# Kernel optimization log

Measured on AMD Instinct MI355X. Metric: run time of the kernel, lower is better.

The kernel has to match this reference:

```python
import jax, jax.numpy as jnp
import numpy as np

N, D = 8192, 2
MIN_DIST = 0.1


def setup_inputs() -> dict:
    key = jax.random.key(0)
    k1, k2 = jax.random.split(key)
    predictions = jax.random.uniform(k1, (N, D), dtype=jnp.float32)
    targets = jax.random.uniform(k2, (N, D), dtype=jnp.float32)
    return {"predictions": predictions, "targets": targets}


def reference(predictions, targets):
    # primary loss: MSE (mean reduction), matching nn.MSELoss / F.mse_loss default
    primary_loss = jnp.mean(jnp.square(predictions - targets))

    # pairwise Euclidean distances via ||pi||^2 + ||pj||^2 - 2 pi.pj
    sq = jnp.sum(jnp.square(predictions), axis=-1)          # [N]
    d2 = sq[:, None] + sq[None, :] - 2.0 * (predictions @ predictions.T)  # [N, N]

    # only pairs with i < j contribute (strict upper triangle)
    mask = jnp.triu(jnp.ones((N, N), dtype=bool), k=1)
    d2 = jnp.where(mask, jnp.maximum(d2, 0.0), 1.0)  # dummy 1.0 keeps sqrt grad-safe
    dist = jnp.sqrt(d2)

    # penalty: (min_distance - d)^2 when d < min_distance, else 0
    pen = jnp.square(jnp.maximum(MIN_DIST - dist, 0.0))
    proximity_penalty = jnp.sum(jnp.where(mask, pen, 0.0))

    return primary_loss + proximity_penalty
```

## Files before the change

kernel.cpp:

```cpp
#include <hip/hip_runtime.h>

#define NPTS 8192
#define TILE 128
#define TT (NPTS / TILE)
#define NPAIRS (TT * (TT + 1) / 2)
#define MIN_DIST 0.1f

__global__ __launch_bounds__(64) void pair_tiles(const float2* __restrict__ P,
                                                 const float* __restrict__ pred,
                                                 const float* __restrict__ targ,
                                                 float* __restrict__ partial) {
    int k = blockIdx.x;

    int bi = (int)(((float)(2 * TT + 1) -
                    sqrtf((float)((2 * TT + 1) * (2 * TT + 1) - 8 * k))) * 0.5f);
    bi = min(max(bi, 0), TT - 1);
    while (bi > 0 && (bi * TT - bi * (bi - 1) / 2) > k) --bi;
    while (((bi + 1) * TT - (bi + 1) * bi / 2) <= k) ++bi;
    int bj = bi + (k - (bi * TT - bi * (bi - 1) / 2));
    bi = __builtin_amdgcn_readfirstlane(bi);
    bj = __builtin_amdgcn_readfirstlane(bj);

    int t = threadIdx.x;
    float2 a0 = P[bi * TILE + t];
    float2 a1 = P[bi * TILE + 64 + t];
    const float4* __restrict__ q4 = (const float4*)(P + bj * TILE);

    float acc = 0.0f;
    if (bi == bj) {
#pragma unroll 8
        for (int jj = 0; jj < TILE / 2; ++jj) {
            float4 q = q4[jj];
            float dx0 = a0.x - q.x, dy0 = a0.y - q.y;
            float dx1 = a0.x - q.z, dy1 = a0.y - q.w;
            float dx2 = a1.x - q.x, dy2 = a1.y - q.y;
            float dx3 = a1.x - q.z, dy3 = a1.y - q.w;
            float u0 = fmaxf(MIN_DIST - __builtin_amdgcn_sqrtf(fmaf(dy0, dy0, dx0 * dx0)), 0.0f);
            float u1 = fmaxf(MIN_DIST - __builtin_amdgcn_sqrtf(fmaf(dy1, dy1, dx1 * dx1)), 0.0f);
            float u2 = fmaxf(MIN_DIST - __builtin_amdgcn_sqrtf(fmaf(dy2, dy2, dx2 * dx2)), 0.0f);
            float u3 = fmaxf(MIN_DIST - __builtin_amdgcn_sqrtf(fmaf(dy3, dy3, dx3 * dx3)), 0.0f);
            u0 = (2 * jj == t) ? 0.0f : u0;
            u1 = (2 * jj + 1 == t) ? 0.0f : u1;
            u2 = (2 * jj == 64 + t) ? 0.0f : u2;
            u3 = (2 * jj + 1 == 64 + t) ? 0.0f : u3;
            acc = fmaf(u0, u0, acc);
            acc = fmaf(u1, u1, acc);
            acc = fmaf(u2, u2, acc);
            acc = fmaf(u3, u3, acc);
        }
        acc *= 0.5f;
    } else {
#pragma unroll 8
        for (int jj = 0; jj < TILE / 2; ++jj) {
            float4 q = q4[jj];
            float dx0 = a0.x - q.x, dy0 = a0.y - q.y;
            float dx1 = a0.x - q.z, dy1 = a0.y - q.w;
            float dx2 = a1.x - q.x, dy2 = a1.y - q.y;
            float dx3 = a1.x - q.z, dy3 = a1.y - q.w;
            float u0 = fmaxf(MIN_DIST - __builtin_amdgcn_sqrtf(fmaf(dy0, dy0, dx0 * dx0)), 0.0f);
            float u1 = fmaxf(MIN_DIST - __builtin_amdgcn_sqrtf(fmaf(dy1, dy1, dx1 * dx1)), 0.0f);
            float u2 = fmaxf(MIN_DIST - __builtin_amdgcn_sqrtf(fmaf(dy2, dy2, dx2 * dx2)), 0.0f);
            float u3 = fmaxf(MIN_DIST - __builtin_amdgcn_sqrtf(fmaf(dy3, dy3, dx3 * dx3)), 0.0f);
            acc = fmaf(u0, u0, acc);
            acc = fmaf(u1, u1, acc);
            acc = fmaf(u2, u2, acc);
            acc = fmaf(u3, u3, acc);
        }
    }

    if (k < 32) {
        int base = k * 128 + t;
        float4 p0 = ((const float4*)pred)[base];
        float4 r0 = ((const float4*)targ)[base];
        float4 p1 = ((const float4*)pred)[base + 64];
        float4 r1 = ((const float4*)targ)[base + 64];
        float e0 = p0.x - r0.x, e1 = p0.y - r0.y, e2 = p0.z - r0.z, e3 = p0.w - r0.w;
        float e4 = p1.x - r1.x, e5 = p1.y - r1.y, e6 = p1.z - r1.z, e7 = p1.w - r1.w;
        float m = e0 * e0;
        m = fmaf(e1, e1, m);
        m = fmaf(e2, e2, m);
        m = fmaf(e3, e3, m);
        m = fmaf(e4, e4, m);
        m = fmaf(e5, e5, m);
        m = fmaf(e6, e6, m);
        m = fmaf(e7, e7, m);
        acc = fmaf(m, 1.0f / 16384.0f, acc);
    }

    for (int off = 32; off > 0; off >>= 1)
        acc += __shfl_down(acc, off, 64);
    if (t == 0) partial[k] = acc;
}

__global__ __launch_bounds__(256) void finalize(const float* __restrict__ partial,
                                                float* __restrict__ out) {
    int t = threadIdx.x;
    double s = 0.0;
    for (int i = t; i < NPAIRS; i += 256) s += (double)partial[i];

    for (int off = 32; off > 0; off >>= 1) s += __shfl_down(s, off, 64);
    __shared__ double sm[4];
    if ((t & 63) == 0) sm[t >> 6] = s;
    __syncthreads();
    if (t == 0) out[0] = (float)(sm[0] + sm[1] + sm[2] + sm[3]);
}

extern "C" void kernel_launch(void* const* d_in, const int* in_sizes, int n_in,
                              void* d_out, int out_size, void* d_ws, size_t ws_size,
                              hipStream_t stream) {
    const float* pred = (const float*)d_in[0];
    const float* targ = (const float*)d_in[1];
    float* partial = (float*)d_ws;

    pair_tiles<<<NPAIRS, 64, 0, stream>>>((const float2*)pred, pred, targ, partial);
    finalize<<<1, 256, 0, stream>>>(partial, (float*)d_out);
}
```

Measured before the change: 71.03 us.

## Use 256-point tiles with 4-wave blocks and readlane broadcast of column points

Tile size grows from 128 to 256, and each block now has 4 waves. Each wave covers 64 column points against 256 row points held in registers. Column coordinates are broadcast with readlane instead of being loaded through memory as float4 per iteration. This cuts block count and removes per-iteration global/L1 loads, but adds a shared-memory cross-wave reduction, a diagonal masking branch inside the loop, and fewer blocks (528) for load balance across CUs.

```diff
diff --git a/kernel.cpp b/kernel.cpp
--- a/kernel.cpp
+++ b/kernel.cpp
@@ -1,95 +1,87 @@
 #include <hip/hip_runtime.h>
 
 #define NPTS 8192
-#define TILE 128
-#define TT (NPTS / TILE)
-#define NPAIRS (TT * (TT + 1) / 2)
+#define TILE 256
+#define NT (NPTS / TILE)
+#define NPAIRS (NT * (NT + 1) / 2)
 #define MIN_DIST 0.1f
 
-__global__ __launch_bounds__(64) void pair_tiles(const float2* __restrict__ P,
-                                                 const float* __restrict__ pred,
-                                                 const float* __restrict__ targ,
-                                                 float* __restrict__ partial) {
+__device__ __forceinline__ float bcast(float v, int lane) {
+    return __uint_as_float(__builtin_amdgcn_readlane(__float_as_uint(v), (unsigned)lane));
+}
+
+__global__ __launch_bounds__(256) void pair_tiles(const float2* __restrict__ P,
+                                                  const float* __restrict__ pred,
+                                                  const float* __restrict__ targ,
+                                                  float* __restrict__ partial) {
     int k = blockIdx.x;
 
-    int bi = (int)(((float)(2 * TT + 1) -
-                    sqrtf((float)((2 * TT + 1) * (2 * TT + 1) - 8 * k))) * 0.5f);
-    bi = min(max(bi, 0), TT - 1);
-    while (bi > 0 && (bi * TT - bi * (bi - 1) / 2) > k) --bi;
-    while (((bi + 1) * TT - (bi + 1) * bi / 2) <= k) ++bi;
-    int bj = bi + (k - (bi * TT - bi * (bi - 1) / 2));
+    int bi = (int)(((float)(2 * NT + 1) -
+                    sqrtf((float)((2 * NT + 1) * (2 * NT + 1) - 8 * k))) * 0.5f);
+    bi = min(max(bi, 0), NT - 1);
+    while (bi > 0 && (bi * NT - bi * (bi - 1) / 2) > k) --bi;
+    while (((bi + 1) * NT - (bi + 1) * bi / 2) <= k) ++bi;
+    int bj = bi + (k - (bi * NT - bi * (bi - 1) / 2));
     bi = __builtin_amdgcn_readfirstlane(bi);
     bj = __builtin_amdgcn_readfirstlane(bj);
 
-    int t = threadIdx.x;
-    float2 a0 = P[bi * TILE + t];
-    float2 a1 = P[bi * TILE + 64 + t];
-    const float4* __restrict__ q4 = (const float4*)(P + bj * TILE);
+    int tid = threadIdx.x;
+    int w = tid >> 6;
+    int l = tid & 63;
 
+    float2 a0 = P[bi * TILE + l];
+    float2 a1 = P[bi * TILE + 64 + l];
+    float2 a2 = P[bi * TILE + 128 + l];
+    float2 a3 = P[bi * TILE + 192 + l];
+    float2 pj = P[bj * TILE + w * 64 + l];
+
+    bool diag = (bi == bj);
     float acc = 0.0f;
-    if (bi == bj) {
+
 #pragma unroll 8
-        for (int jj = 0; jj < TILE / 2; ++jj) {
-            float4 q = q4[jj];
-            float dx0 = a0.x - q.x, dy0 = a0.y - q.y;
-            float dx1 = a0.x - q.z, dy1 = a0.y - q.w;
-            float dx2 = a1.x - q.x, dy2 = a1.y - q.y;
-            float dx3 = a1.x - q.z, dy3 = a1.y - q.w;
-            float u0 = fmaxf(MIN_DIST - __builtin_amdgcn_sqrtf(fmaf(dy0, dy0, dx0 * dx0)), 0.0f);
-            float u1 = fmaxf(MIN_DIST - __builtin_amdgcn_sqrtf(fmaf(dy1, dy1, dx1 * dx1)), 0.0f);
-            float u2 = fmaxf(MIN_DIST - __builtin_amdgcn_sqrtf(fmaf(dy2, dy2, dx2 * dx2)), 0.0f);
-            float u3 = fmaxf(MIN_DIST - __builtin_amdgcn_sqrtf(fmaf(dy3, dy3, dx3 * dx3)), 0.0f);
-            u0 = (2 * jj == t) ? 0.0f : u0;
-            u1 = (2 * jj + 1 == t) ? 0.0f : u1;
-            u2 = (2 * jj == 64 + t) ? 0.0f : u2;
-            u3 = (2 * jj + 1 == 64 + t) ? 0.0f : u3;
-            acc = fmaf(u0, u0, acc);
-            acc = fmaf(u1, u1, acc);
-            acc = fmaf(u2, u2, acc);
-            acc = fmaf(u3, u3, acc);
+    for (int s = 0; s < 64; ++s) {
+        float qx = bcast(pj.x, s);
+        float qy = bcast(pj.y, s);
+
+        float dx0 = a0.x - qx, dy0 = a0.y - qy;
+        float dx1 = a1.x - qx, dy1 = a1.y - qy;
+        float dx2 = a2.x - qx, dy2 = a2.y - qy;
+        float dx3 = a3.x - qx, dy3 = a3.y - qy;
+        float u0 = fmaxf(MIN_DIST - __builtin_amdgcn_sqrtf(fmaf(dy0, dy0, dx0 * dx0)), 0.0f);
+        float u1 = fmaxf(MIN_DIST - __builtin_amdgcn_sqrtf(fmaf(dy1, dy1, dx1 * dx1)), 0.0f);
+        float u2 = fmaxf(MIN_DIST - __builtin_amdgcn_sqrtf(fmaf(dy2, dy2, dx2 * dx2)), 0.0f);
+        float u3 = fmaxf(MIN_DIST - __builtin_amdgcn_sqrtf(fmaf(dy3, dy3, dx3 * dx3)), 0.0f);
+        if (diag) {
+            if (w == 0) u0 = (l == s) ? 0.0f : u0;
+            if (w == 1) u1 = (l == s) ? 0.0f : u1;
+            if (w == 2) u2 = (l == s) ? 0.0f : u2;
+            if (w == 3) u3 = (l == s) ? 0.0f : u3;
         }
-        acc *= 0.5f;
-    } else {
-#pragma unroll 8
-        for (int jj = 0; jj < TILE / 2; ++jj) {
-            float4 q = q4[jj];
-            float dx0 = a0.x - q.x, dy0 = a0.y - q.y;
-            float dx1 = a0.x - q.z, dy1 = a0.y - q.w;
-            float dx2 = a1.x - q.x, dy2 = a1.y - q.y;
-            float dx3 = a1.x - q.z, dy3 = a1.y - q.w;
-            float u0 = fmaxf(MIN_DIST - __builtin_amdgcn_sqrtf(fmaf(dy0, dy0, dx0 * dx0)), 0.0f);
-            float u1 = fmaxf(MIN_DIST - __builtin_amdgcn_sqrtf(fmaf(dy1, dy1, dx1 * dx1)), 0.0f);
-            float u2 = fmaxf(MIN_DIST - __builtin_amdgcn_sqrtf(fmaf(dy2, dy2, dx2 * dx2)), 0.0f);
-            float u3 = fmaxf(MIN_DIST - __builtin_amdgcn_sqrtf(fmaf(dy3, dy3, dx3 * dx3)), 0.0f);
-            acc = fmaf(u0, u0, acc);
-            acc = fmaf(u1, u1, acc);
-            acc = fmaf(u2, u2, acc);
-            acc = fmaf(u3, u3, acc);
-        }
+        acc = fmaf(u0, u0, acc);
+        acc = fmaf(u1, u1, acc);
+        acc = fmaf(u2, u2, acc);
+        acc = fmaf(u3, u3, acc);
     }
+    if (diag) acc *= 0.5f;
 
-    if (k < 32) {
-        int base = k * 128 + t;
-        float4 p0 = ((const float4*)pred)[base];
-        float4 r0 = ((const float4*)targ)[base];
-        float4 p1 = ((const float4*)pred)[base + 64];
-        float4 r1 = ((const float4*)targ)[base + 64];
-        float e0 = p0.x - r0.x, e1 = p0.y - r0.y, e2 = p0.z - r0.z, e3 = p0.w - r0.w;
-        float e4 = p1.x - r1.x, e5 = p1.y - r1.y, e6 = p1.z - r1.z, e7 = p1.w - r1.w;
+    if (k < 16) {
+        int idx = k * 256 + tid;
+        float4 p = ((const float4*)pred)[idx];
+        float4 t = ((const float4*)targ)[idx];
+        float e0 = p.x - t.x, e1 = p.y - t.y, e2 = p.z - t.z, e3 = p.w - t.w;
         float m = e0 * e0;
         m = fmaf(e1, e1, m);
         m = fmaf(e2, e2, m);
         m = fmaf(e3, e3, m);
-        m = fmaf(e4, e4, m);
-        m = fmaf(e5, e5, m);
-        m = fmaf(e6, e6, m);
-        m = fmaf(e7, e7, m);
         acc = fmaf(m, 1.0f / 16384.0f, acc);
     }
 
     for (int off = 32; off > 0; off >>= 1)
         acc += __shfl_down(acc, off, 64);
-    if (t == 0) partial[k] = acc;
+    __shared__ float wsum[4];
+    if (l == 0) wsum[w] = acc;
+    __syncthreads();
+    if (tid == 0) partial[k] = wsum[0] + wsum[1] + wsum[2] + wsum[3];
 }
 
 __global__ __launch_bounds__(256) void finalize(const float* __restrict__ partial,
@@ -112,6 +104,6 @@
     const float* targ = (const float*)d_in[1];
     float* partial = (float*)d_ws;
 
-    pair_tiles<<<NPAIRS, 64, 0, stream>>>((const float2*)pred, pred, targ, partial);
+    pair_tiles<<<NPAIRS, 256, 0, stream>>>((const float2*)pred, pred, targ, partial);
     finalize<<<1, 256, 0, stream>>>(partial, (float*)d_out);
 }
```

Result: no change. 70.95 us (-0.1%).
